# Kernel tuning notes

Hardware: AMD Instinct MI355X
Metric: run time of the kernel (lower is better)

The kernel has to match this reference:

```python
import jax, jax.numpy as jnp
import numpy as np

N_QUBITS = 4
N_LAYERS = 2


def _apply_1q(state, gate, wire):
    # state: [B,2,2,2,2] complex; gate: [2,2] or [B,2,2] complex
    ax = wire + 1
    st = jnp.moveaxis(state, ax, 1)  # [B,2,...]
    if gate.ndim == 2:
        st = jnp.einsum('ij,bj...->bi...', gate, st)
    else:
        st = jnp.einsum('bij,bj...->bi...', gate, st)
    return jnp.moveaxis(st, 1, ax)


def _cnot(state, control, target):
    ca, ta = control + 1, target + 1
    s0 = jnp.take(state, 0, axis=ca)
    s1 = jnp.take(state, 1, axis=ca)
    ta2 = ta - 1 if ta > ca else ta  # axis shift after take
    s1 = jnp.flip(s1, axis=ta2)      # flip target when control=1
    return jnp.stack([s0, s1], axis=ca)


def _rx(theta):  # theta: [B] -> [B,2,2]
    c = jnp.cos(theta / 2).astype(jnp.complex64)
    s = jnp.sin(theta / 2).astype(jnp.complex64)
    return jnp.stack([jnp.stack([c, -1j * s], -1),
                      jnp.stack([-1j * s, c], -1)], -2)


def _ry(theta):  # scalar -> [2,2]
    c = jnp.cos(theta / 2).astype(jnp.complex64)
    s = jnp.sin(theta / 2).astype(jnp.complex64)
    return jnp.stack([jnp.stack([c, -s]), jnp.stack([s, c])])


def _rz(theta):  # scalar -> [2,2] diag(e^{-i t/2}, e^{i t/2})
    half = (theta / 2).astype(jnp.complex64)
    z = jnp.zeros((), jnp.complex64)
    return jnp.stack([jnp.stack([jnp.exp(-1j * half), z]),
                      jnp.stack([z, jnp.exp(1j * half)])])


def _circuit(angles, wq):
    # angles: [B,4] float32; wq: [2,4,3] float32 -> [B,4] expval PauliZ
    B = angles.shape[0]
    state = jnp.zeros((B, 2, 2, 2, 2), jnp.complex64)
    state = state.at[:, 0, 0, 0, 0].set(1.0)
    for i in range(N_QUBITS):
        state = _apply_1q(state, _rx(angles[:, i]), i)
    for layer in range(N_LAYERS):
        for i in range(N_QUBITS):
            state = _apply_1q(state, _rz(wq[layer, i, 0]), i)
            state = _apply_1q(state, _ry(wq[layer, i, 1]), i)
            state = _apply_1q(state, _rz(wq[layer, i, 2]), i)
        for i in range(N_QUBITS - 1):
            state = _cnot(state, i, i + 1)
    probs = state.real ** 2 + state.imag ** 2  # [B,2,2,2,2]
    zs = []
    for i in range(N_QUBITS):
        axes = tuple(a for a in range(1, 5) if a != i + 1)
        marg = jnp.sum(probs, axis=axes)  # [B,2]
        zs.append(marg[:, 0] - marg[:, 1])
    return jnp.stack(zs, axis=-1)  # [B,4]


def setup_inputs() -> dict:
    key = jax.random.key(0)
    ks = jax.random.split(key, 8)
    B, F = 262144, 64
    x = jax.random.normal(ks[0], (B, F), jnp.float32)
    Wp = jax.random.normal(ks[1], (N_QUBITS, F), jnp.float32) * (1.0 / np.sqrt(F))
    bp = jnp.zeros((N_QUBITS,), jnp.float32)
    wq = 0.01 * jax.random.normal(ks[2], (N_LAYERS, N_QUBITS, 3), jnp.float32)
    W1 = jax.random.normal(ks[3], (64, N_QUBITS), jnp.float32) * 0.5
    b1 = jnp.zeros((64,), jnp.float32)
    W2 = jax.random.normal(ks[4], (1, 64), jnp.float32) * 0.125
    b2 = jnp.zeros((1,), jnp.float32)
    return {"x": x, "Wp": Wp, "bp": bp, "wq": wq, "W1": W1, "b1": b1, "W2": W2, "b2": b2}


def reference(x, Wp, bp, wq, W1, b1, W2, b2):
    angles = x @ Wp.T + bp               # feature_projector -> [B,4]
    q_out = _circuit(angles, wq)         # [B,4]
    h = jax.nn.relu(q_out @ W1.T + b1)   # [B,64]
    return h @ W2.T + b2                 # [B,1]
```

## Files before the change

### kernel.cpp

```cpp
#include <hip/hip_runtime.h>
#include <hip/hip_bf16.h>

#define CBUF_N 1157


__device__ inline void gate_rz(float* ar, float* ai, int q, float th) {
    float c = cosf(0.5f * th), s = sinf(0.5f * th);
    int st = 8 >> q;
    #pragma unroll
    for (int k = 0; k < 16; k++) {
        float r = ar[k], im = ai[k];
        if (k & st) {
            ar[k] = r * c - im * s;
            ai[k] = im * c + r * s;
        } else {
            ar[k] = r * c + im * s;
            ai[k] = im * c - r * s;
        }
    }
}

__device__ inline void gate_ry(float* ar, float* ai, int q, float th) {
    float c = cosf(0.5f * th), s = sinf(0.5f * th);
    int st = 8 >> q;
    #pragma unroll
    for (int k = 0; k < 16; k++) {
        if (!(k & st)) {
            int k1 = k | st;
            float r0 = ar[k], i0 = ai[k], r1 = ar[k1], i1 = ai[k1];
            ar[k]  = c * r0 - s * r1;  ai[k]  = c * i0 - s * i1;
            ar[k1] = s * r0 + c * r1;  ai[k1] = s * i0 + c * i1;
        }
    }
}

__device__ inline void gate_cnot(float* ar, float* ai, int c, int t) {
    int stc = 8 >> c, stt = 8 >> t;
    #pragma unroll
    for (int k = 0; k < 16; k++) {
        if ((k & stc) && !(k & stt)) {
            int k1 = k | stt;
            float r = ar[k], im = ai[k];
            ar[k] = ar[k1]; ai[k] = ai[k1];
            ar[k1] = r;     ai[k1] = im;
        }
    }
}

__global__ void precompute_kernel(const float* __restrict__ Wp,
                                  const float* __restrict__ bp,
                                  const float* __restrict__ wq,
                                  const float* __restrict__ W1,
                                  const float* __restrict__ b1,
                                  const float* __restrict__ W2,
                                  const float* __restrict__ b2,
                                  float* __restrict__ ws) {
    int t = threadIdx.x;

    if (t < 16) {
        float ar[16], ai[16];
        #pragma unroll
        for (int k = 0; k < 16; k++) { ar[k] = 0.f; ai[k] = 0.f; }
        ar[t] = 1.f;

        for (int layer = 0; layer < 2; layer++) {
            for (int q = 0; q < 4; q++) {
                const float* w = &wq[(layer * 4 + q) * 3];
                gate_rz(ar, ai, q, w[0]);
                gate_ry(ar, ai, q, w[1]);
                gate_rz(ar, ai, q, w[2]);
            }
            for (int c = 0; c < 3; c++) gate_cnot(ar, ai, c, c + 1);
        }

        int pc = __popc(t) & 3;
        #pragma unroll
        for (int j = 0; j < 16; j++) {
            float re = ar[j], im = ai[j], vr, vi;
            switch (pc) {
                case 0: vr = re;  vi = im;  break;
                case 1: vr = im;  vi = -re; break;
                case 2: vr = -re; vi = -im; break;
                case 3: vr = -im; vi = re;  break;
            }
            ws[j * 16 + t]       = vr;
            ws[256 + j * 16 + t] = vi;
        }
    }

    for (int q = 0; q < 4; q++) ws[512 + t * 4 + q] = Wp[q * 64 + t];
    if (t < 4) ws[768 + t] = bp[t];

    ws[772 + t * 6 + 0] = W1[t * 4 + 0];
    ws[772 + t * 6 + 1] = W1[t * 4 + 1];
    ws[772 + t * 6 + 2] = W1[t * 4 + 2];
    ws[772 + t * 6 + 3] = W1[t * 4 + 3];
    ws[772 + t * 6 + 4] = b1[t];
    ws[772 + t * 6 + 5] = W2[t];
    if (t == 0) ws[1156] = b2[0];
}


__global__ __launch_bounds__(256) void qmain_kernel(const float* __restrict__ x,
                                                    const float* __restrict__ cb,
                                                    float* __restrict__ out,
                                                    int B) {
    __shared__ float tile[256 * 33];
    const int t = threadIdx.x;
    const long row0 = (long)blockIdx.x * 256;
    const float* xb = x + row0 * 64;

    float ang[4];
    #pragma unroll
    for (int q = 0; q < 4; q++) ang[q] = cb[768 + q];

    #pragma unroll
    for (int s = 0; s < 2; s++) {
        if (s) __syncthreads();
        #pragma unroll
        for (int r = 0; r < 8; r++) {
            int idx = r * 1024 + t * 4;
            int row = idx >> 5;
            int col = idx & 31;
            float4 v = *reinterpret_cast<const float4*>(xb + row * 64 + s * 32 + col);
            float* dst = &tile[row * 33 + col];
            dst[0] = v.x; dst[1] = v.y; dst[2] = v.z; dst[3] = v.w;
        }
        __syncthreads();
        const float* myrow = &tile[t * 33];
        #pragma unroll
        for (int i = 0; i < 32; i++) {
            float xv = myrow[i];
            const float* w = &cb[512 + (s * 32 + i) * 4];
            #pragma unroll
            for (int q = 0; q < 4; q++) ang[q] = fmaf(xv, w[q], ang[q]);
        }
    }

    float c[4], s4[4];
    #pragma unroll
    for (int q = 0; q < 4; q++) {
        __sincosf(0.5f * ang[q], &s4[q], &c[q]);
    }
    float pre[4]  = { c[0] * c[1], c[0] * s4[1], s4[0] * c[1], s4[0] * s4[1] };
    float post[4] = { c[2] * c[3], c[2] * s4[3], s4[2] * c[3], s4[2] * s4[3] };
    float m[16];
    #pragma unroll
    for (int k = 0; k < 16; k++) m[k] = pre[k >> 2] * post[k & 3];

    float z0 = 0.f, z1 = 0.f, z2 = 0.f, z3 = 0.f;
    #pragma unroll
    for (int j = 0; j < 16; j++) {
        const float* vr = &cb[j * 16];
        const float* vi = &cb[256 + j * 16];
        float re = 0.f, im = 0.f;
        #pragma unroll
        for (int k = 0; k < 16; k++) {
            re = fmaf(vr[k], m[k], re);
            im = fmaf(vi[k], m[k], im);
        }
        float p = re * re + im * im;
        z0 += (j & 8) ? -p : p;
        z1 += (j & 4) ? -p : p;
        z2 += (j & 2) ? -p : p;
        z3 += (j & 1) ? -p : p;
    }

    float acc = cb[1156];
    #pragma unroll
    for (int j = 0; j < 64; j++) {
        const float* mp = &cb[772 + j * 6];
        float h = mp[4];
        h = fmaf(mp[0], z0, h);
        h = fmaf(mp[1], z1, h);
        h = fmaf(mp[2], z2, h);
        h = fmaf(mp[3], z3, h);
        h = fmaxf(h, 0.f);
        acc = fmaf(mp[5], h, acc);
    }
    out[row0 + t] = acc;
}


extern "C" void kernel_launch(void* const* d_in, const int* in_sizes, int n_in,
                              void* d_out, int out_size, void* d_ws, size_t ws_size,
                              hipStream_t stream) {
    const float* x  = (const float*)d_in[0];
    const float* Wp = (const float*)d_in[1];
    const float* bp = (const float*)d_in[2];
    const float* wq = (const float*)d_in[3];
    const float* W1 = (const float*)d_in[4];
    const float* b1 = (const float*)d_in[5];
    const float* W2 = (const float*)d_in[6];
    const float* b2 = (const float*)d_in[7];
    float* ws = (float*)d_ws;
    float* out = (float*)d_out;

    int B = in_sizes[0] / 64;

    precompute_kernel<<<1, 64, 0, stream>>>(Wp, bp, wq, W1, b1, W2, b2, ws);

    int grid = (B + 255) / 256;
    qmain_kernel<<<grid, 256, 0, stream>>>(x, ws, out, B);
}
```

Before: 126.4 us.

## Stage constants in LDS and load x rows directly as float4 per thread

Copies the precomputed constant buffer into shared memory, padded for aligned float4 reads, instead of reading it from global memory as scalars. Each thread now reads its own 64-float row of x with float4 loads rather than staging a transposed tile through shared memory. That removes the two barriers and the padded tile, and raises the occupancy hint. The per-thread row reads are strided by 256 bytes across lanes, so global coalescing is worse and depends on cache behaviour.

```diff
diff --git a/kernel.cpp b/kernel.cpp
--- a/kernel.cpp
+++ b/kernel.cpp
@@ -1,11 +1,12 @@
 #include <hip/hip_runtime.h>
-#include <hip/hip_bf16.h>
-
-#define CBUF_N 1157
+
+#define CB_FLOATS 1292
+#define CB_V4 (CB_FLOATS / 4)
 
 
 __device__ inline void gate_rz(float* ar, float* ai, int q, float th) {
-    float c = cosf(0.5f * th), s = sinf(0.5f * th);
+    float c, s;
+    __sincosf(0.5f * th, &s, &c);
     int st = 8 >> q;
     #pragma unroll
     for (int k = 0; k < 16; k++) {
@@ -21,7 +22,8 @@
 }
 
 __device__ inline void gate_ry(float* ar, float* ai, int q, float th) {
-    float c = cosf(0.5f * th), s = sinf(0.5f * th);
+    float c, s;
+    __sincosf(0.5f * th, &s, &c);
     int st = 8 >> q;
     #pragma unroll
     for (int k = 0; k < 16; k++) {
@@ -90,60 +92,57 @@
 
     for (int q = 0; q < 4; q++) ws[512 + t * 4 + q] = Wp[q * 64 + t];
     if (t < 4) ws[768 + t] = bp[t];
-
-    ws[772 + t * 6 + 0] = W1[t * 4 + 0];
-    ws[772 + t * 6 + 1] = W1[t * 4 + 1];
-    ws[772 + t * 6 + 2] = W1[t * 4 + 2];
-    ws[772 + t * 6 + 3] = W1[t * 4 + 3];
-    ws[772 + t * 6 + 4] = b1[t];
-    ws[772 + t * 6 + 5] = W2[t];
-    if (t == 0) ws[1156] = b2[0];
-}
-
-
-__global__ __launch_bounds__(256) void qmain_kernel(const float* __restrict__ x,
-                                                    const float* __restrict__ cb,
-                                                    float* __restrict__ out,
-                                                    int B) {
-    __shared__ float tile[256 * 33];
+    if (t < 4) ws[772 + t] = 0.f;
+
+    ws[776 + t * 8 + 0] = W1[t * 4 + 0];
+    ws[776 + t * 8 + 1] = W1[t * 4 + 1];
+    ws[776 + t * 8 + 2] = W1[t * 4 + 2];
+    ws[776 + t * 8 + 3] = W1[t * 4 + 3];
+    ws[776 + t * 8 + 4] = b1[t];
+    ws[776 + t * 8 + 5] = W2[t];
+    ws[776 + t * 8 + 6] = 0.f;
+    ws[776 + t * 8 + 7] = 0.f;
+    if (t == 0) { ws[1288] = b2[0]; ws[1289] = 0.f; ws[1290] = 0.f; ws[1291] = 0.f; }
+}
+
+
+__global__ __launch_bounds__(256, 4) void qmain_kernel(const float* __restrict__ x,
+                                                       const float* __restrict__ cb,
+                                                       float* __restrict__ out,
+                                                       int B) {
+    __shared__ __align__(16) float w[CB_FLOATS];
     const int t = threadIdx.x;
-    const long row0 = (long)blockIdx.x * 256;
-    const float* xb = x + row0 * 64;
-
-    float ang[4];
-    #pragma unroll
-    for (int q = 0; q < 4; q++) ang[q] = cb[768 + q];
-
-    #pragma unroll
-    for (int s = 0; s < 2; s++) {
-        if (s) __syncthreads();
-        #pragma unroll
-        for (int r = 0; r < 8; r++) {
-            int idx = r * 1024 + t * 4;
-            int row = idx >> 5;
-            int col = idx & 31;
-            float4 v = *reinterpret_cast<const float4*>(xb + row * 64 + s * 32 + col);
-            float* dst = &tile[row * 33 + col];
-            dst[0] = v.x; dst[1] = v.y; dst[2] = v.z; dst[3] = v.w;
-        }
-        __syncthreads();
-        const float* myrow = &tile[t * 33];
-        #pragma unroll
-        for (int i = 0; i < 32; i++) {
-            float xv = myrow[i];
-            const float* w = &cb[512 + (s * 32 + i) * 4];
-            #pragma unroll
-            for (int q = 0; q < 4; q++) ang[q] = fmaf(xv, w[q], ang[q]);
-        }
-    }
-
-    float c[4], s4[4];
-    #pragma unroll
-    for (int q = 0; q < 4; q++) {
-        __sincosf(0.5f * ang[q], &s4[q], &c[q]);
-    }
-    float pre[4]  = { c[0] * c[1], c[0] * s4[1], s4[0] * c[1], s4[0] * s4[1] };
-    float post[4] = { c[2] * c[3], c[2] * s4[3], s4[2] * c[3], s4[2] * s4[3] };
+    {
+        float4* dst = reinterpret_cast<float4*>(w);
+        const float4* src = reinterpret_cast<const float4*>(cb);
+        for (int i = t; i < CB_V4; i += 256) dst[i] = src[i];
+    }
+    __syncthreads();
+
+    const int row = blockIdx.x * 256 + t;
+    if (row >= B) return;
+
+    const float4* __restrict__ xr = reinterpret_cast<const float4*>(x + (size_t)row * 64);
+
+    float ang0 = w[768], ang1 = w[769], ang2 = w[770], ang3 = w[771];
+    #pragma unroll 4
+    for (int i = 0; i < 16; i++) {
+        float4 v = xr[i];
+        const float4* wt = reinterpret_cast<const float4*>(&w[512 + i * 16]);
+        float4 w0 = wt[0], w1 = wt[1], w2 = wt[2], w3 = wt[3];
+        ang0 = fmaf(v.x, w0.x, fmaf(v.y, w1.x, fmaf(v.z, w2.x, fmaf(v.w, w3.x, ang0))));
+        ang1 = fmaf(v.x, w0.y, fmaf(v.y, w1.y, fmaf(v.z, w2.y, fmaf(v.w, w3.y, ang1))));
+        ang2 = fmaf(v.x, w0.z, fmaf(v.y, w1.z, fmaf(v.z, w2.z, fmaf(v.w, w3.z, ang2))));
+        ang3 = fmaf(v.x, w0.w, fmaf(v.y, w1.w, fmaf(v.z, w2.w, fmaf(v.w, w3.w, ang3))));
+    }
+
+    float c0, s0, c1, s1, c2, s2, c3, s3;
+    __sincosf(0.5f * ang0, &s0, &c0);
+    __sincosf(0.5f * ang1, &s1, &c1);
+    __sincosf(0.5f * ang2, &s2, &c2);
+    __sincosf(0.5f * ang3, &s3, &c3);
+    float pre[4]  = { c0 * c1, c0 * s1, s0 * c1, s0 * s1 };
+    float post[4] = { c2 * c3, c2 * s3, s2 * c3, s2 * s3 };
     float m[16];
     #pragma unroll
     for (int k = 0; k < 16; k++) m[k] = pre[k >> 2] * post[k & 3];
@@ -151,13 +150,21 @@
     float z0 = 0.f, z1 = 0.f, z2 = 0.f, z3 = 0.f;
     #pragma unroll
     for (int j = 0; j < 16; j++) {
-        const float* vr = &cb[j * 16];
-        const float* vi = &cb[256 + j * 16];
+        const float4* vr = reinterpret_cast<const float4*>(&w[j * 16]);
+        const float4* vi = reinterpret_cast<const float4*>(&w[256 + j * 16]);
         float re = 0.f, im = 0.f;
         #pragma unroll
-        for (int k = 0; k < 16; k++) {
-            re = fmaf(vr[k], m[k], re);
-            im = fmaf(vi[k], m[k], im);
+        for (int k4 = 0; k4 < 4; k4++) {
+            float4 a = vr[k4];
+            float4 b = vi[k4];
+            re = fmaf(a.x, m[4 * k4 + 0], re);
+            re = fmaf(a.y, m[4 * k4 + 1], re);
+            re = fmaf(a.z, m[4 * k4 + 2], re);
+            re = fmaf(a.w, m[4 * k4 + 3], re);
+            im = fmaf(b.x, m[4 * k4 + 0], im);
+            im = fmaf(b.y, m[4 * k4 + 1], im);
+            im = fmaf(b.z, m[4 * k4 + 2], im);
+            im = fmaf(b.w, m[4 * k4 + 3], im);
         }
         float p = re * re + im * im;
         z0 += (j & 8) ? -p : p;
@@ -166,19 +173,16 @@
         z3 += (j & 1) ? -p : p;
     }
 
-    float acc = cb[1156];
+    float acc = w[1288];
     #pragma unroll
     for (int j = 0; j < 64; j++) {
-        const float* mp = &cb[772 + j * 6];
-        float h = mp[4];
-        h = fmaf(mp[0], z0, h);
-        h = fmaf(mp[1], z1, h);
-        h = fmaf(mp[2], z2, h);
-        h = fmaf(mp[3], z3, h);
+        float4 a  = *reinterpret_cast<const float4*>(&w[776 + j * 8]);
+        float2 bb = *reinterpret_cast<const float2*>(&w[776 + j * 8 + 4]);
+        float h = fmaf(a.x, z0, fmaf(a.y, z1, fmaf(a.z, z2, fmaf(a.w, z3, bb.x))));
         h = fmaxf(h, 0.f);
-        acc = fmaf(mp[5], h, acc);
-    }
-    out[row0 + t] = acc;
+        acc = fmaf(bb.y, h, acc);
+    }
+    out[row] = acc;
 }
 
 
```

Measured after the change: 123.9 us. -2.0%, faster.
